# Performance work log

Measured on AMD Instinct MI355X. Metric: run time of the kernel, lower is better.

## Reference

```python
import jax, jax.numpy as jnp
import numpy as np

VOCAB = 2          # len(CHAR_VOCAB) in source
CE = 16            # char_embed_dim
CNN_OUT = 32 + 64 + 128  # 224
EMBED = 64


def _conv1d(x, w, b, pad):
    # x: [N, Cin, L]; w: [Cout, Cin, K]; torch Conv1d semantics
    y = jax.lax.conv_general_dilated(
        x, w, window_strides=(1,), padding=[(pad, pad)],
        dimension_numbers=('NCH', 'OIH', 'NCH'))
    return y + b[None, :, None]


def setup_inputs() -> dict:
    key = jax.random.key(0)
    ks = jax.random.split(key, 12)
    B, S, MC = 32, 2048, 20
    char_ids = jax.random.randint(ks[0], (B, S, MC), 0, VOCAB, dtype=jnp.int64)
    E = jax.random.normal(ks[1], (VOCAB, CE), jnp.float32)
    E = E.at[0].set(0.0)  # padding_idx=0
    s = 0.05
    return {
        'char_ids': char_ids,
        'E': E,
        'W1': jax.random.normal(ks[2], (32, CE, 1), jnp.float32) * s,
        'b1': jnp.zeros((32,), jnp.float32),
        'W2': jax.random.normal(ks[3], (64, CE, 2), jnp.float32) * s,
        'b2': jnp.zeros((64,), jnp.float32),
        'W3': jax.random.normal(ks[4], (128, CE, 3), jnp.float32) * s,
        'b3': jnp.zeros((128,), jnp.float32),
        'Ht_W': jax.random.normal(ks[5], (CNN_OUT, CNN_OUT), jnp.float32) * s,
        'Ht_b': jnp.zeros((CNN_OUT,), jnp.float32),
        'Hg_W': jax.random.normal(ks[6], (CNN_OUT, CNN_OUT), jnp.float32) * s,
        'Hg_b': jnp.zeros((CNN_OUT,), jnp.float32),
        'P_W': jax.random.normal(ks[7], (EMBED, CNN_OUT), jnp.float32) * s,
        'P_b': jnp.zeros((EMBED,), jnp.float32),
    }


def reference(char_ids, E, W1, b1, W2, b2, W3, b3, Ht_W, Ht_b, Hg_W, Hg_b, P_W, P_b):
    B, S, MC = char_ids.shape
    ids = char_ids.reshape(-1, MC)                      # [N, MC]
    emb = E[ids]                                        # [N, MC, CE]
    x = jnp.transpose(emb, (0, 2, 1))                   # [N, CE, MC]
    p1 = jnp.max(jax.nn.relu(_conv1d(x, W1, b1, 0)), axis=2)  # [N, 32]
    p2 = jnp.max(jax.nn.relu(_conv1d(x, W2, b2, 1)), axis=2)  # [N, 64]
    p3 = jnp.max(jax.nn.relu(_conv1d(x, W3, b3, 1)), axis=2)  # [N, 128]
    cnn = jnp.concatenate([p1, p2, p3], axis=1)         # [N, 224]
    t = jax.nn.relu(cnn @ Ht_W.T + Ht_b)
    g = jax.nn.sigmoid(cnn @ Hg_W.T + Hg_b)
    hw = g * t + (1.0 - g) * cnn
    out = hw @ P_W.T + P_b                              # [N, 64]
    return out.reshape(B, S, -1)
```

## Files before the change

kernel.cpp:

```cpp
#include <hip/hip_runtime.h>


typedef _Float16 f16;
typedef __attribute__((ext_vector_type(8))) _Float16 f16x8;
typedef __attribute__((ext_vector_type(4))) float f32x4;

#define LC1   0
#define LRAW2 96
#define LT2   672
#define LRAW3 1696
#define LT3LO 5152
#define LT3HI 7200
#define TABSZ 9248
#define NKEYS 4096
#define CROW  232
#define UOUT_OFF 0

__device__ __forceinline__ f16x8 hmax8(f16x8 a, f16x8 b) {
  return __builtin_elementwise_max(a, b);
}

__device__ __forceinline__ f16x8 pin8(f16x8 v) {
  union { f16x8 v; unsigned w[4]; } x; x.v = v;
  asm volatile("" : "+v"(x.w[0]), "+v"(x.w[1]), "+v"(x.w[2]), "+v"(x.w[3]) :: "memory");
  return x.v;
}

union RegA {
  struct { float X[3][16]; float U1[3][32]; float U2[9][64]; float U3[27][128]; } u;
  f16 wstage[4 * 16 * CROW];
};

__device__ __forceinline__ void stage_slice(const float* __restrict__ src,
                                            f16* wst, int lane, int LO) {
  const f32x4* s4 = (const f32x4*)src;
#pragma unroll
  for (int i = 0; i < 14; i++) {
    int idx = i * 64 + lane;
    int flat = idx * 4;
    int r = flat / 224, c = flat - r * 224;
    f32x4 v = s4[idx];
    union { f16 h[4]; unsigned u2[2]; } o;
    if (LO) {
      o.h[0] = (f16)(v[0] - (float)(f16)v[0]); o.h[1] = (f16)(v[1] - (float)(f16)v[1]);
      o.h[2] = (f16)(v[2] - (float)(f16)v[2]); o.h[3] = (f16)(v[3] - (float)(f16)v[3]);
    } else {
      o.h[0] = (f16)v[0]; o.h[1] = (f16)v[1]; o.h[2] = (f16)v[2]; o.h[3] = (f16)v[3];
    }
    *(uint2*)&wst[r * CROW + c] = *(uint2*)o.u2;
  }
}

__global__ __launch_bounds__(256) void ucompute_kernel(
    const float* __restrict__ E,
    const float* __restrict__ W1, const float* __restrict__ b1,
    const float* __restrict__ W2, const float* __restrict__ b2,
    const float* __restrict__ W3, const float* __restrict__ b3,
    const float* __restrict__ HtW, const float* __restrict__ HgW,
    const float* __restrict__ PW,
    const float* __restrict__ Htb, const float* __restrict__ Hgb,
    const float* __restrict__ Pb, float* __restrict__ uout)
{
  __shared__ RegA ra;
  __shared__ __attribute__((aligned(16))) f16 tab[TABSZ];
  __shared__ __attribute__((aligned(16))) f16 cnn[16 * CROW];

  const int tid = threadIdx.x;
  const int bid = blockIdx.x;
  const int wave = tid >> 6, lane = tid & 63;
  const int kbase = bid * 16;
  const int lrow = lane & 15;
  const int kg8 = (lane >> 4) * 8;
  const int rr0 = (lane >> 4) * 4;

  if (tid < 48) { int s = tid >> 4, i = tid & 15; ra.u.X[s][i] = (s == 0) ? 0.f : E[(s - 1) * 16 + i]; }
  __syncthreads();
  for (int idx = tid; idx < 96; idx += 256) {
    int s = idx >> 5, c = idx & 31;
    float acc = b1[c];
#pragma unroll
    for (int i = 0; i < 16; i++) acc += W1[c * 16 + i] * ra.u.X[s][i];
    ra.u.U1[s][c] = acc;
  }
  for (int idx = tid; idx < 576; idx += 256) {
    int p = idx >> 6, c = idx & 63;
    int sa = p / 3, sb = p % 3;
    float acc = b2[c];
#pragma unroll
    for (int i = 0; i < 16; i++)
      acc += W2[c * 32 + i * 2 + 0] * ra.u.X[sa][i] + W2[c * 32 + i * 2 + 1] * ra.u.X[sb][i];
    ra.u.U2[p][c] = acc;
  }
  for (int idx = tid; idx < 3456; idx += 256) {
    int p = idx >> 7, c = idx & 127;
    int sa = p / 9, sb = (p / 3) % 3, sc = p % 3;
    float acc = b3[c];
#pragma unroll
    for (int i = 0; i < 16; i++)
      acc += W3[c * 48 + i * 3 + 0] * ra.u.X[sa][i]
           + W3[c * 48 + i * 3 + 1] * ra.u.X[sb][i]
           + W3[c * 48 + i * 3 + 2] * ra.u.X[sc][i];
    ra.u.U3[p][c] = acc;
  }
  __syncthreads();

  if (tid < 96) {
    int r = tid >> 5, c = tid & 31;
    float v = (r == 0) ? fmaxf(ra.u.U1[1][c], ra.u.U1[2][c]) : ra.u.U1[r][c];
    tab[LC1 + tid] = (f16)v;
  }
  for (int idx = tid; idx < 576; idx += 256) tab[LRAW2 + idx] = (f16)ra.u.U2[idx >> 6][idx & 63];
  for (int idx = tid; idx < 3456; idx += 256) tab[LRAW3 + idx] = (f16)ra.u.U3[idx >> 7][idx & 127];
  for (int idx = tid; idx < 1024; idx += 256) {
    int s = idx >> 6, c = idx & 63;
    float m = -65504.f;
#pragma unroll
    for (int b = 0; b < 4; b++)
      if ((s >> b) & 1) m = fmaxf(m, ra.u.U2[4 + 3 * (b >> 1) + (b & 1)][c]);
    tab[LT2 + idx] = (f16)m;
  }
  for (int idx = tid; idx < 2048; idx += 256) {
    int s = idx >> 7, c = idx & 127;
    float m = -65504.f;
#pragma unroll
    for (int b = 0; b < 4; b++)
      if ((s >> b) & 1) m = fmaxf(m, ra.u.U3[13 + 3 * (b >> 1) + (b & 1)][c]);
    tab[LT3LO + idx] = (f16)m;
    m = -65504.f;
#pragma unroll
    for (int b = 0; b < 4; b++)
      if ((s >> b) & 1) m = fmaxf(m, ra.u.U3[22 + 3 * (b >> 1) + (b & 1)][c]);
    tab[LT3HI + idx] = (f16)m;
  }
  __syncthreads();

  const int p1row = tid >> 4;
  const int p1g = tid & 15;
  unsigned mw, mb;
  {
    unsigned key = (unsigned)(kbase + p1row);
    unsigned m3i = key & 255u;
    int st1 = 1 + (int)((key >> 8) & 1),  st2 = 1 + (int)((key >> 9) & 1);
    int st19 = 1 + (int)((key >> 10) & 1), st20 = 1 + (int)((key >> 11) & 1);
    unsigned m2i = 0, mchar = 0;
#pragma unroll
    for (int p = 0; p < 8; p++)
      if ((m3i >> p) & 1) {
        m2i |= (1u << (p >> 1)) | (1u << (p & 3));
        mchar |= (1u << ((p >> 2) & 1)) | (1u << ((p >> 1) & 1)) | (1u << (p & 1));
      }
    unsigned sel = (mchar == 3u) ? 0u : ((mchar & 1u) ? 1u : 2u);
    mw = m3i | (m2i << 8) | (sel << 12);
    mb = (unsigned)st1 | ((unsigned)(st20 * 3) << 4)
       | ((unsigned)(st1 * 3 + st2) << 8) | ((unsigned)(st19 * 9 + st20 * 3) << 16);
  }
  const f16x8 KZ = {0, 0, 0, 0, 0, 0, 0, 0};
  {
    const int m3 = mw & 255;
    f16x8 v = hmax8(*(const f16x8*)&tab[LT3LO + (m3 & 15) * 128 + p1g * 8],
                    *(const f16x8*)&tab[LT3HI + ((m3 >> 4) & 15) * 128 + p1g * 8]);
    v = hmax8(v, *(const f16x8*)&tab[LRAW3 + ((mb >> 8) & 15) * 128 + p1g * 8]);
    v = hmax8(v, *(const f16x8*)&tab[LRAW3 + ((mb >> 16) & 31) * 128 + p1g * 8]);
    *(f16x8*)&cnn[p1row * CROW + 96 + p1g * 8] = hmax8(v, KZ);
    if (p1g < 8) {
      f16x8 u = *(const f16x8*)&tab[LT2 + ((mw >> 8) & 15) * 64 + p1g * 8];
      u = hmax8(u, *(const f16x8*)&tab[LRAW2 + (mb & 15) * 64 + p1g * 8]);
      u = hmax8(u, *(const f16x8*)&tab[LRAW2 + ((mb >> 4) & 15) * 64 + p1g * 8]);
      *(f16x8*)&cnn[p1row * CROW + 32 + p1g * 8] = hmax8(u, KZ);
    }
    if (p1g < 4) {
      int sel = (mw >> 12) & 3;
      f16x8 w = *(const f16x8*)&tab[LC1 + sel * 32 + p1g * 8];
      *(f16x8*)&cnn[p1row * CROW + p1g * 8] = hmax8(w, KZ);
    }
  }
  __syncthreads();

  f16x8 af[7];
#pragma unroll
  for (int kf = 0; kf < 7; kf++)
    af[kf] = *(const f16x8*)&cnn[lrow * CROW + kf * 32 + kg8];
#pragma unroll
  for (int kf = 0; kf < 7; kf++) af[kf] = pin8(af[kf]);
  __syncthreads();

  f16* wst = &ra.wstage[wave * 16 * CROW];

  const int nf_cnt = (wave < 2) ? 4 : 3;
  for (int i = 0; i < nf_cnt; i++) {
    const int nf = wave + i * 4;
    const int col = nf * 16 + lrow;
    const float bt = Htb[col], bg = Hgb[col];
    f32x4 aT = {bt, bt, bt, bt};
    f32x4 aG = {bg, bg, bg, bg};
    stage_slice(HtW + (size_t)nf * 16 * 224, wst, lane, 0);
#pragma unroll
    for (int kf = 0; kf < 7; kf++)
      aT = __builtin_amdgcn_mfma_f32_16x16x32_f16(
          af[kf], *(const f16x8*)&wst[lrow * CROW + kf * 32 + kg8], aT, 0, 0, 0);
    stage_slice(HgW + (size_t)nf * 16 * 224, wst, lane, 0);
#pragma unroll
    for (int kf = 0; kf < 7; kf++)
      aG = __builtin_amdgcn_mfma_f32_16x16x32_f16(
          af[kf], *(const f16x8*)&wst[lrow * CROW + kf * 32 + kg8], aG, 0, 0, 0);
#pragma unroll
    for (int r = 0; r < 4; r++) {
      int row = rr0 + r;
      float t  = fmaxf(aT[r], 0.f);
      float gg = __builtin_amdgcn_rcpf(1.f + __expf(-aG[r]));
      float cv = (float)cnn[row * CROW + col];
      cnn[row * CROW + col] = (f16)(cv + gg * (t - cv));
    }
  }
  __syncthreads();

  f16x8 ah[7];
#pragma unroll
  for (int kf = 0; kf < 7; kf++)
    ah[kf] = *(const f16x8*)&cnn[lrow * CROW + kf * 32 + kg8];
  {
    const int col = wave * 16 + lrow;
    const float bp = Pb[col];
    f32x4 ac = {bp, bp, bp, bp};
    stage_slice(PW + (size_t)wave * 16 * 224, wst, lane, 0);
#pragma unroll
    for (int kf = 0; kf < 7; kf++)
      ac = __builtin_amdgcn_mfma_f32_16x16x32_f16(
          ah[kf], *(const f16x8*)&wst[lrow * CROW + kf * 32 + kg8], ac, 0, 0, 0);
    stage_slice(PW + (size_t)wave * 16 * 224, wst, lane, 1);
#pragma unroll
    for (int kf = 0; kf < 7; kf++)
      ac = __builtin_amdgcn_mfma_f32_16x16x32_f16(
          ah[kf], *(const f16x8*)&wst[lrow * CROW + kf * 32 + kg8], ac, 0, 0, 0);
#pragma unroll
    for (int r = 0; r < 4; r++)
      uout[(size_t)(kbase + rr0 + r) * 64 + col] = ac[r];
  }
}

__global__ __launch_bounds__(256) void keyscatter_kernel(
    const int* __restrict__ ids, const float* __restrict__ uout,
    float* __restrict__ out, int n_tok)
{
  __shared__ unsigned keys[64];
  const int tid = threadIdx.x;
  const int tok0 = blockIdx.x * 64;

  if (tid < 64) {
    unsigned key = 0;
    int t = tok0 + tid;
    if (t < n_tok) {
      const int4* idp4 = (const int4*)(ids + (size_t)t * 20);
      int st[21];
#pragma unroll
      for (int q = 0; q < 5; q++) {
        int4 v = idp4[q];
        st[q * 4 + 1] = v.x; st[q * 4 + 2] = v.y;
        st[q * 4 + 3] = v.z; st[q * 4 + 4] = v.w;
      }
      unsigned m3i = 0;
#pragma unroll
      for (int l = 1; l <= 18; l++)
        m3i |= 1u << ((st[l] << 2) | (st[l + 1] << 1) | st[l + 2]);
      key = m3i | ((unsigned)st[1] << 8) | ((unsigned)st[2] << 9)
          | ((unsigned)st[19] << 10) | ((unsigned)st[20] << 11);
    }
    keys[tid] = key;
  }
  __syncthreads();

  const int tl = tid >> 2, q = tid & 3;
  const int t = tok0 + tl;
  if (t >= n_tok) return;
  const f32x4* src = (const f32x4*)(uout + (size_t)keys[tl] * 64 + q * 16);
  f32x4 v0 = src[0], v1 = src[1], v2 = src[2], v3 = src[3];
  f32x4* dst = (f32x4*)(out + (size_t)t * 64 + q * 16);
  dst[0] = v0; dst[1] = v1; dst[2] = v2; dst[3] = v3;
}

extern "C" void kernel_launch(void* const* d_in, const int* in_sizes, int n_in,
                              void* d_out, int out_size, void* d_ws, size_t ws_size,
                              hipStream_t stream) {
  const int*   ids = (const int*)d_in[0];
  const float* E   = (const float*)d_in[1];
  const float* W1  = (const float*)d_in[2];
  const float* b1  = (const float*)d_in[3];
  const float* W2  = (const float*)d_in[4];
  const float* b2  = (const float*)d_in[5];
  const float* W3  = (const float*)d_in[6];
  const float* b3  = (const float*)d_in[7];
  const float* HtW = (const float*)d_in[8];
  const float* Htb = (const float*)d_in[9];
  const float* HgW = (const float*)d_in[10];
  const float* Hgb = (const float*)d_in[11];
  const float* PW  = (const float*)d_in[12];
  const float* Pb  = (const float*)d_in[13];
  float* out = (float*)d_out;
  float* uout = (float*)((char*)d_ws + UOUT_OFF);
  const int n_tok = in_sizes[0] / 20;

  ucompute_kernel<<<NKEYS / 16, 256, 0, stream>>>(
      E, W1, b1, W2, b2, W3, b3, HtW, HgW, PW, Htb, Hgb, Pb, uout);
  keyscatter_kernel<<<(n_tok + 63) / 64, 256, 0, stream>>>(ids, uout, out, n_tok);
}
```

Baseline: 32.39 us.

## Compute conv lookup tables once in a separate kernel instead of per block

```diff
diff --git a/kernel.cpp b/kernel.cpp
--- a/kernel.cpp
+++ b/kernel.cpp
@@ -14,7 +14,7 @@
 #define TABSZ 9248
 #define NKEYS 4096
 #define CROW  232
-#define UOUT_OFF 0
+#define UOUT_OFF 20480
 
 __device__ __forceinline__ f16x8 hmax8(f16x8 a, f16x8 b) {
   return __builtin_elementwise_max(a, b);
@@ -26,10 +26,114 @@
   return x.v;
 }
 
-union RegA {
-  struct { float X[3][16]; float U1[3][32]; float U2[9][64]; float U3[27][128]; } u;
-  f16 wstage[4 * 16 * CROW];
-};
+__device__ __forceinline__ float xs(const float* __restrict__ E, int s, int i) {
+  return (s == 0) ? 0.f : E[(s - 1) * 16 + i];
+}
+
+__global__ __launch_bounds__(256) void lut_kernel(
+    const float* __restrict__ E,
+    const float* __restrict__ W1, const float* __restrict__ b1,
+    const float* __restrict__ W2, const float* __restrict__ b2,
+    const float* __restrict__ W3, const float* __restrict__ b3,
+    f16* __restrict__ tab)
+{
+  const int tid = threadIdx.x;
+  const int bid = blockIdx.x;
+
+  if (bid < 27) {
+    if (tid >= 128) return;
+    const int c = tid, p = bid;
+    const int sa = p / 9, sb = (p / 3) % 3, sc = p % 3;
+    const float* w = W3 + c * 48;
+    float acc = b3[c];
+#pragma unroll
+    for (int i = 0; i < 16; i++)
+      acc += w[i * 3 + 0] * xs(E, sa, i) + w[i * 3 + 1] * xs(E, sb, i)
+           + w[i * 3 + 2] * xs(E, sc, i);
+    tab[LRAW3 + p * 128 + c] = (f16)acc;
+    return;
+  }
+  if (bid < 43) {
+    if (tid >= 128) return;
+    const int c = tid, s = bid - 27;
+    const float* w = W3 + c * 48;
+    float lo = -65504.f, hi = -65504.f;
+#pragma unroll
+    for (int b = 0; b < 4; b++) {
+      if (!((s >> b) & 1)) continue;
+      int pl = 13 + 3 * (b >> 1) + (b & 1);
+      int ph = 22 + 3 * (b >> 1) + (b & 1);
+      int sal = pl / 9, sbl = (pl / 3) % 3, scl = pl % 3;
+      int sah = ph / 9, sbh = (ph / 3) % 3, sch = ph % 3;
+      float al = b3[c], ah = b3[c];
+#pragma unroll
+      for (int i = 0; i < 16; i++) {
+        al += w[i * 3 + 0] * xs(E, sal, i) + w[i * 3 + 1] * xs(E, sbl, i)
+            + w[i * 3 + 2] * xs(E, scl, i);
+        ah += w[i * 3 + 0] * xs(E, sah, i) + w[i * 3 + 1] * xs(E, sbh, i)
+            + w[i * 3 + 2] * xs(E, sch, i);
+      }
+      lo = fmaxf(lo, al);
+      hi = fmaxf(hi, ah);
+    }
+    tab[LT3LO + s * 128 + c] = (f16)lo;
+    tab[LT3HI + s * 128 + c] = (f16)hi;
+    return;
+  }
+  if (bid == 43) {
+    const int c = tid & 63, part = tid >> 6;
+    const float* w = W2 + c * 32;
+    if (part < 2) {
+      int p0 = part * 5;
+      int pend = part ? 9 : 5;
+      for (int p = p0; p < pend; p++) {
+        int sa = p / 3, sb = p % 3;
+        float acc = b2[c];
+#pragma unroll
+        for (int i = 0; i < 16; i++)
+          acc += w[i * 2 + 0] * xs(E, sa, i) + w[i * 2 + 1] * xs(E, sb, i);
+        tab[LRAW2 + p * 64 + c] = (f16)acc;
+      }
+    } else {
+      float u[4];
+#pragma unroll
+      for (int b = 0; b < 4; b++) {
+        int p = 4 + 3 * (b >> 1) + (b & 1);
+        int sa = p / 3, sb = p % 3;
+        float acc = b2[c];
+#pragma unroll
+        for (int i = 0; i < 16; i++)
+          acc += w[i * 2 + 0] * xs(E, sa, i) + w[i * 2 + 1] * xs(E, sb, i);
+        u[b] = acc;
+      }
+      int s0 = (part - 2) * 8;
+#pragma unroll
+      for (int j = 0; j < 8; j++) {
+        int s = s0 + j;
+        float m = -65504.f;
+#pragma unroll
+        for (int b = 0; b < 4; b++)
+          if ((s >> b) & 1) m = fmaxf(m, u[b]);
+        tab[LT2 + s * 64 + c] = (f16)m;
+      }
+    }
+    return;
+  }
+  {
+    if (tid >= 32) return;
+    const int c = tid;
+    const float* w = W1 + c * 16;
+    float u1 = b1[c], u2 = b1[c];
+#pragma unroll
+    for (int i = 0; i < 16; i++) {
+      u1 += w[i] * E[i];
+      u2 += w[i] * E[16 + i];
+    }
+    tab[LC1 + 0 * 32 + c] = (f16)fmaxf(u1, u2);
+    tab[LC1 + 1 * 32 + c] = (f16)u1;
+    tab[LC1 + 2 * 32 + c] = (f16)u2;
+  }
+}
 
 __device__ __forceinline__ void stage_slice(const float* __restrict__ src,
                                             f16* wst, int lane, int LO) {
@@ -52,18 +156,14 @@
 }
 
 __global__ __launch_bounds__(256) void ucompute_kernel(
-    const float* __restrict__ E,
-    const float* __restrict__ W1, const float* __restrict__ b1,
-    const float* __restrict__ W2, const float* __restrict__ b2,
-    const float* __restrict__ W3, const float* __restrict__ b3,
+    const f16* __restrict__ tab,
     const float* __restrict__ HtW, const float* __restrict__ HgW,
     const float* __restrict__ PW,
     const float* __restrict__ Htb, const float* __restrict__ Hgb,
     const float* __restrict__ Pb, float* __restrict__ uout)
 {
-  __shared__ RegA ra;
-  __shared__ __attribute__((aligned(16))) f16 tab[TABSZ];
   __shared__ __attribute__((aligned(16))) f16 cnn[16 * CROW];
+  __shared__ __attribute__((aligned(16))) f16 wstage[4 * 16 * CROW];
 
   const int tid = threadIdx.x;
   const int bid = blockIdx.x;
@@ -72,67 +172,6 @@
   const int lrow = lane & 15;
   const int kg8 = (lane >> 4) * 8;
   const int rr0 = (lane >> 4) * 4;
-
-  if (tid < 48) { int s = tid >> 4, i = tid & 15; ra.u.X[s][i] = (s == 0) ? 0.f : E[(s - 1) * 16 + i]; }
-  __syncthreads();
-  for (int idx = tid; idx < 96; idx += 256) {
-    int s = idx >> 5, c = idx & 31;
-    float acc = b1[c];
-#pragma unroll
-    for (int i = 0; i < 16; i++) acc += W1[c * 16 + i] * ra.u.X[s][i];
-    ra.u.U1[s][c] = acc;
-  }
-  for (int idx = tid; idx < 576; idx += 256) {
-    int p = idx >> 6, c = idx & 63;
-    int sa = p / 3, sb = p % 3;
-    float acc = b2[c];
-#pragma unroll
-    for (int i = 0; i < 16; i++)
-      acc += W2[c * 32 + i * 2 + 0] * ra.u.X[sa][i] + W2[c * 32 + i * 2 + 1] * ra.u.X[sb][i];
-    ra.u.U2[p][c] = acc;
-  }
-  for (int idx = tid; idx < 3456; idx += 256) {
-    int p = idx >> 7, c = idx & 127;
-    int sa = p / 9, sb = (p / 3) % 3, sc = p % 3;
-    float acc = b3[c];
-#pragma unroll
-    for (int i = 0; i < 16; i++)
-      acc += W3[c * 48 + i * 3 + 0] * ra.u.X[sa][i]
-           + W3[c * 48 + i * 3 + 1] * ra.u.X[sb][i]
-           + W3[c * 48 + i * 3 + 2] * ra.u.X[sc][i];
-    ra.u.U3[p][c] = acc;
-  }
-  __syncthreads();
-
-  if (tid < 96) {
-    int r = tid >> 5, c = tid & 31;
-    float v = (r == 0) ? fmaxf(ra.u.U1[1][c], ra.u.U1[2][c]) : ra.u.U1[r][c];
-    tab[LC1 + tid] = (f16)v;
-  }
-  for (int idx = tid; idx < 576; idx += 256) tab[LRAW2 + idx] = (f16)ra.u.U2[idx >> 6][idx & 63];
-  for (int idx = tid; idx < 3456; idx += 256) tab[LRAW3 + idx] = (f16)ra.u.U3[idx >> 7][idx & 127];
-  for (int idx = tid; idx < 1024; idx += 256) {
-    int s = idx >> 6, c = idx & 63;
-    float m = -65504.f;
-#pragma unroll
-    for (int b = 0; b < 4; b++)
-      if ((s >> b) & 1) m = fmaxf(m, ra.u.U2[4 + 3 * (b >> 1) + (b & 1)][c]);
-    tab[LT2 + idx] = (f16)m;
-  }
-  for (int idx = tid; idx < 2048; idx += 256) {
-    int s = idx >> 7, c = idx & 127;
-    float m = -65504.f;
-#pragma unroll
-    for (int b = 0; b < 4; b++)
-      if ((s >> b) & 1) m = fmaxf(m, ra.u.U3[13 + 3 * (b >> 1) + (b & 1)][c]);
-    tab[LT3LO + idx] = (f16)m;
-    m = -65504.f;
-#pragma unroll
-    for (int b = 0; b < 4; b++)
-      if ((s >> b) & 1) m = fmaxf(m, ra.u.U3[22 + 3 * (b >> 1) + (b & 1)][c]);
-    tab[LT3HI + idx] = (f16)m;
-  }
-  __syncthreads();
 
   const int p1row = tid >> 4;
   const int p1g = tid & 15;
@@ -154,23 +193,24 @@
     mb = (unsigned)st1 | ((unsigned)(st20 * 3) << 4)
        | ((unsigned)(st1 * 3 + st2) << 8) | ((unsigned)(st19 * 9 + st20 * 3) << 16);
   }
+
   const f16x8 KZ = {0, 0, 0, 0, 0, 0, 0, 0};
   {
     const int m3 = mw & 255;
-    f16x8 v = hmax8(*(const f16x8*)&tab[LT3LO + (m3 & 15) * 128 + p1g * 8],
-                    *(const f16x8*)&tab[LT3HI + ((m3 >> 4) & 15) * 128 + p1g * 8]);
-    v = hmax8(v, *(const f16x8*)&tab[LRAW3 + ((mb >> 8) & 15) * 128 + p1g * 8]);
-    v = hmax8(v, *(const f16x8*)&tab[LRAW3 + ((mb >> 16) & 31) * 128 + p1g * 8]);
+    f16x8 v = hmax8(*(const f16x8*)(tab + LT3LO + (m3 & 15) * 128 + p1g * 8),
+                    *(const f16x8*)(tab + LT3HI + ((m3 >> 4) & 15) * 128 + p1g * 8));
+    v = hmax8(v, *(const f16x8*)(tab + LRAW3 + ((mb >> 8) & 15) * 128 + p1g * 8));
+    v = hmax8(v, *(const f16x8*)(tab + LRAW3 + ((mb >> 16) & 31) * 128 + p1g * 8));
     *(f16x8*)&cnn[p1row * CROW + 96 + p1g * 8] = hmax8(v, KZ);
     if (p1g < 8) {
-      f16x8 u = *(const f16x8*)&tab[LT2 + ((mw >> 8) & 15) * 64 + p1g * 8];
-      u = hmax8(u, *(const f16x8*)&tab[LRAW2 + (mb & 15) * 64 + p1g * 8]);
-      u = hmax8(u, *(const f16x8*)&tab[LRAW2 + ((mb >> 4) & 15) * 64 + p1g * 8]);
+      f16x8 u = *(const f16x8*)(tab + LT2 + ((mw >> 8) & 15) * 64 + p1g * 8);
+      u = hmax8(u, *(const f16x8*)(tab + LRAW2 + (mb & 15) * 64 + p1g * 8));
+      u = hmax8(u, *(const f16x8*)(tab + LRAW2 + ((mb >> 4) & 15) * 64 + p1g * 8));
       *(f16x8*)&cnn[p1row * CROW + 32 + p1g * 8] = hmax8(u, KZ);
     }
     if (p1g < 4) {
       int sel = (mw >> 12) & 3;
-      f16x8 w = *(const f16x8*)&tab[LC1 + sel * 32 + p1g * 8];
+      f16x8 w = *(const f16x8*)(tab + LC1 + sel * 32 + p1g * 8);
       *(f16x8*)&cnn[p1row * CROW + p1g * 8] = hmax8(w, KZ);
     }
   }
@@ -184,7 +224,7 @@
   for (int kf = 0; kf < 7; kf++) af[kf] = pin8(af[kf]);
   __syncthreads();
 
-  f16* wst = &ra.wstage[wave * 16 * CROW];
+  f16* wst = &wstage[wave * 16 * CROW];
 
   const int nf_cnt = (wave < 2) ? 4 : 3;
   for (int i = 0; i < nf_cnt; i++) {
@@ -296,10 +336,13 @@
   const float* PW  = (const float*)d_in[12];
   const float* Pb  = (const float*)d_in[13];
   float* out = (float*)d_out;
-  float* uout = (float*)((char*)d_ws + UOUT_OFF);
+  char* ws = (char*)d_ws;
+  f16* tab = (f16*)ws;
+  float* uout = (float*)(ws + UOUT_OFF);
   const int n_tok = in_sizes[0] / 20;
 
+  lut_kernel<<<45, 256, 0, stream>>>(E, W1, b1, W2, b2, W3, b3, tab);
   ucompute_kernel<<<NKEYS / 16, 256, 0, stream>>>(
-      E, W1, b1, W2, b2, W3, b3, HtW, HgW, PW, Htb, Hgb, Pb, uout);
+      tab, HtW, HgW, PW, Htb, Hgb, Pb, uout);
   keyscatter_kernel<<<(n_tok + 63) / 64, 256, 0, stream>>>(ids, uout, out, n_tok);
 }
```

Result: slower. 37.61 us (+16.1%).
